# Kernel tuning notes

Hardware: AMD Instinct MI355X
Metric: run time of the kernel (lower is better)

## Reference

```python
import jax, jax.numpy as jnp
import numpy as np

B, TOK, NT = 64, 64, 456          # batch, token_encoder_dim, num gene tokens
T = NT * TOK                      # flat gene_exp dim = 29184
D, H, NL = 256, 8, 4              # d_model, nhead, num_layers
HD = D // H                       # head_dim = 32
FF = 4 * D                        # ffn hidden
PH = 32                           # attention-pooling hidden
L = NT + 1                        # seq len incl. CLS token
LN_EPS = 1e-5
BN_EPS = 1e-5


def build_alibi_slopes(n_heads):
    # faithful to FlashAttentionBlock.build_alibi_slopes (base=2.0)
    return jnp.array([1.0 / 2.0 ** (i // (n_heads / 2.0)) for i in range(n_heads)],
                     dtype=jnp.float32)


def _ln(x, g, b):
    m = jnp.mean(x, axis=-1, keepdims=True)
    v = jnp.mean(jnp.square(x - m), axis=-1, keepdims=True)
    return (x - m) * jax.lax.rsqrt(v + LN_EPS) * g + b


def setup_inputs() -> dict:
    key = jax.random.key(0)
    ks = jax.random.split(key, 24)
    s = 0.02
    return {
        "gene_exp": jax.random.normal(ks[0], (B, T), dtype=jnp.float32),
        "coords": jax.random.normal(ks[1], (B, 3), dtype=jnp.float32),
        "w_in": jax.random.normal(ks[2], (TOK, D)) * s,
        "b_in": jnp.zeros((D,), jnp.float32),
        "w_cls": jax.random.normal(ks[3], (3, D)) * s,
        "b_cls": jnp.zeros((D,), jnp.float32),
        "qkv_w": jax.random.normal(ks[4], (NL, D, 3 * D)) * s,
        "qkv_b": jnp.zeros((NL, 3 * D), jnp.float32),
        "ln1_g": jnp.ones((NL, D), jnp.float32),
        "ln1_b": jnp.zeros((NL, D), jnp.float32),
        "ffn_w1": jax.random.normal(ks[5], (NL, D, FF)) * s,
        "ffn_b1": jnp.zeros((NL, FF), jnp.float32),
        "ffn_w2": jax.random.normal(ks[6], (NL, FF, D)) * s,
        "ffn_b2": jnp.zeros((NL, D), jnp.float32),
        "ln2_g": jnp.ones((NL, D), jnp.float32),
        "ln2_b": jnp.zeros((NL, D), jnp.float32),
        "th1_w": jax.random.normal(ks[7], (D, PH)) * s,
        "th1_b": jnp.zeros((PH,), jnp.float32),
        "bn_g": jnp.ones((PH,), jnp.float32),
        "bn_b": jnp.zeros((PH,), jnp.float32),
        "th2_w": jax.random.normal(ks[8], (PH, 1)) * s,
        "th2_b": jnp.zeros((1,), jnp.float32),
    }


def reference(gene_exp, coords, w_in, b_in, w_cls, b_cls, qkv_w, qkv_b,
              ln1_g, ln1_b, ffn_w1, ffn_b1, ffn_w2, ffn_b2, ln2_g, ln2_b,
              th1_w, th1_b, bn_g, bn_b, th2_w, th2_b):
    # tokenize gene expression + project
    x = gene_exp.reshape(B, NT, TOK) @ w_in + b_in            # [B, NT, D]
    cls = (coords @ w_cls + b_cls)[:, None, :]                # [B, 1, D]
    x = jnp.concatenate([cls, x], axis=1)                     # [B, L, D]

    # ALiBi bias: -slope_h * |i - j| (non-causal flash-attn convention)
    slopes = build_alibi_slopes(H)                            # [H]
    pos = jnp.arange(L, dtype=jnp.float32)
    bias = -slopes[:, None, None] * jnp.abs(pos[:, None] - pos[None, :])  # [H,L,L]

    scale = 1.0 / np.sqrt(HD)
    for l in range(NL):
        residual = x
        qkv = (x @ qkv_w[l] + qkv_b[l]).reshape(B, L, 3, H, HD)
        q, k, v = qkv[:, :, 0], qkv[:, :, 1], qkv[:, :, 2]    # [B, L, H, HD]
        scores = jnp.einsum('bihd,bjhd->bhij', q, k) * scale + bias
        attn = jax.nn.softmax(scores, axis=-1)                # [B, H, L, L]
        out = jnp.einsum('bhij,bjhd->bihd', attn, v).reshape(B, L, D)
        x = _ln(residual + out, ln1_g[l], ln1_b[l])
        residual = x
        h = jax.nn.relu(x @ ffn_w1[l] + ffn_b1[l]) @ ffn_w2[l] + ffn_b2[l]
        x = _ln(residual + h, ln2_g[l], ln2_b[l])

    # AttentionPooling (BatchNorm1d in eval mode: running mean 0, var 1)
    h = x @ th1_w + th1_b                                     # [B, L, PH]
    h = h * (bn_g / np.sqrt(1.0 + BN_EPS)) + bn_b
    scores = jax.nn.gelu(h) @ th2_w + th2_b                   # [B, L, 1]
    attn_w = jax.nn.softmax(scores, axis=1)[..., 0]           # [B, L]
    pooled = jnp.einsum('bl,bld->bd', attn_w, x)              # [B, D]
    return pooled
```

## Files before the change

kernel.cpp:

```cpp
#include <hip/hip_runtime.h>
#include <math.h>

#define B_   64
#define TOK_ 64
#define NT_  456
#define L_   457
#define D_   256
#define H_   8
#define HD_  32
#define FF_  1024
#define NL_  4
#define PH_  32
#define MPAD 29312

typedef unsigned int uint;
typedef unsigned short ushort;
typedef __bf16 v8bf __attribute__((ext_vector_type(8)));
typedef __bf16 v4bf __attribute__((ext_vector_type(4)));
typedef short v4s __attribute__((ext_vector_type(4)));
typedef float v4f __attribute__((ext_vector_type(4)));

__device__ __forceinline__ float bu2f(ushort x) {
    return __uint_as_float(((uint)x) << 16);
}
__device__ __forceinline__ ushort f2bu(float f) {
    union { float f; uint u; } x; x.f = f;
    uint r = (x.u + 0x7fffu + ((x.u >> 16) & 1u)) >> 16;
    return (ushort)r;
}
__device__ __forceinline__ uint pack_bf2(float a, float b) {
#if defined(__HIP_DEVICE_COMPILE__) && __has_builtin(__builtin_amdgcn_cvt_pk_bf16_f32)
    typedef __bf16 bf2v __attribute__((ext_vector_type(2)));
    bf2v v = __builtin_amdgcn_cvt_pk_bf16_f32(a, b);
    return *(uint*)&v;
#else
    return (uint)f2bu(a) | ((uint)f2bu(b) << 16);
#endif
}

__device__ __forceinline__ v4f mfma16(uint2 a, uint2 b, v4f c) {
#if defined(__HIP_DEVICE_COMPILE__)
#if __has_builtin(__builtin_amdgcn_mfma_f32_16x16x16_bf16)
    return __builtin_amdgcn_mfma_f32_16x16x16_bf16(*(v4bf*)&a, *(v4bf*)&b, c, 0, 0, 0);
#else
    return __builtin_amdgcn_mfma_f32_16x16x16bf16_1k(*(v4s*)&a, *(v4s*)&b, c, 0, 0, 0);
#endif
#else
    (void)a; (void)b;
    return c;
#endif
}

__device__ __forceinline__ void gload16(const void* g, void* l) {
    __builtin_amdgcn_global_load_lds(
        (const __attribute__((address_space(1))) void*)(unsigned long long)(uintptr_t)g,
        (__attribute__((address_space(3))) void*)(uint)(uintptr_t)l,
        16, 0, 0);
}

__global__ __launch_bounds__(256) void mfma_gemm(
    const ushort* __restrict__ A, const ushort* __restrict__ WT,
    const float* __restrict__ bias, ushort* __restrict__ Cout,
    int N, int K, int relu, int T)
{
    __shared__ ushort lds_all[128 * 132];
    ushort* As = lds_all;
    ushort* Bs = lds_all + 128 * 64;

    int nCB = N >> 7;
    int per = gridDim.x >> 3;
    int lid = blockIdx.x;
    int nlid = (lid & 7) * per + (lid >> 3);
    if (nlid >= T) return;
    int colblk = (nlid % nCB) * 128;
    int rowblk = (nlid / nCB) * 128;

    int tid = threadIdx.x;
    int wave = tid >> 6, lane = tid & 63;
    int wm = wave >> 1, wn = wave & 1;
    int fr = lane & 15, fq = lane >> 4;

    v4f acc[4][4];
#pragma unroll
    for (int i = 0; i < 4; ++i)
#pragma unroll
        for (int j = 0; j < 4; ++j) acc[i][j] = (v4f)0.0f;

    const ushort* Ag[4];
    const ushort* Bg[4];
    ushort* lA[4];
    ushort* lB[4];
#pragma unroll
    for (int p = 0; p < 4; ++p) {
        int c = p * 256 + wave * 64 + lane;
        int r = c >> 3, gs = (c & 7) ^ (r & 7);
        Ag[p] = A + (size_t)(rowblk + r) * K + gs * 8;
        Bg[p] = WT + (size_t)(colblk + r) * K + gs * 8;
        lA[p] = As + (size_t)(p * 256 + wave * 64) * 8;
        lB[p] = Bs + (size_t)(p * 256 + wave * 64) * 8;
    }

    for (int kt = 0; kt < K; kt += 64) {
#pragma unroll
        for (int p = 0; p < 4; ++p) gload16(Ag[p] + kt, lA[p]);
#pragma unroll
        for (int p = 0; p < 4; ++p) gload16(Bg[p] + kt, lB[p]);
        __syncthreads();

#pragma unroll
        for (int ks = 0; ks < 2; ++ks) {
            int pa = (ks * 4 + fq) ^ (fr & 7);
            v8bf a[4], b[4];
#pragma unroll
            for (int mi = 0; mi < 4; ++mi) {
                int rl = wm * 64 + mi * 16 + fr;
                a[mi] = *(const v8bf*)(As + (size_t)(rl * 8 + pa) * 8);
            }
#pragma unroll
            for (int ni = 0; ni < 4; ++ni) {
                int rl = wn * 64 + ni * 16 + fr;
                b[ni] = *(const v8bf*)(Bs + (size_t)(rl * 8 + pa) * 8);
            }
#pragma unroll
            for (int mi = 0; mi < 4; ++mi)
#pragma unroll
                for (int ni = 0; ni < 4; ++ni)
                    acc[mi][ni] = __builtin_amdgcn_mfma_f32_16x16x32_bf16(
                        a[mi], b[ni], acc[mi][ni], 0, 0, 0);
        }
        __syncthreads();
    }

#pragma unroll
    for (int ni = 0; ni < 4; ++ni) {
        int col = wn * 64 + ni * 16 + fr;
        float bv = bias[colblk + col];
#pragma unroll
        for (int mi = 0; mi < 4; ++mi) {
            int row0 = wm * 64 + mi * 16 + fq * 4;
#pragma unroll
            for (int r = 0; r < 4; ++r) {
                float v = acc[mi][ni][r] + bv;
                if (relu) v = fmaxf(v, 0.f);
                lds_all[(size_t)(row0 + r) * 132 + col] = f2bu(v);
            }
        }
    }
    __syncthreads();
#pragma unroll
    for (int i = 0; i < 8; ++i) {
        int u = tid + 256 * i;
        int row = u >> 4, c8 = (u & 15) * 8;
        uint4 val = *(const uint4*)&lds_all[(size_t)row * 132 + c8];
        *(uint4*)(Cout + (size_t)(rowblk + row) * N + colblk + c8) = val;
    }
}

__global__ __launch_bounds__(256) void wcast_kernel(
    const float* __restrict__ W, ushort* __restrict__ WT, int K, int N)
{
    __shared__ float t[32][33];
    const float* Wl = W + (size_t)blockIdx.z * K * N;
    ushort* WTl = WT + (size_t)blockIdx.z * K * N;
    int n0 = blockIdx.x * 32, k0 = blockIdx.y * 32;
    int tx = threadIdx.x, ty = threadIdx.y;
#pragma unroll
    for (int r = 0; r < 32; r += 8)
        t[ty + r][tx] = Wl[(size_t)(k0 + ty + r) * N + n0 + tx];
    __syncthreads();
#pragma unroll
    for (int r = 0; r < 32; r += 8)
        WTl[(size_t)(n0 + ty + r) * K + k0 + tx] = f2bu(t[tx][ty + r]);
}

__global__ __launch_bounds__(256) void sgemm_kernel(
    const float* __restrict__ A, const float* __restrict__ W,
    const float* __restrict__ bias, ushort* __restrict__ Cb,
    int M, int N, int K)
{
    __shared__ float As_[16][64];
    __shared__ float Bs_[16][64];
    int tid = threadIdx.x;
    int rowblk = blockIdx.y * 64;
    int colblk = blockIdx.x * 64;
    int a_row = tid & 63, a_q = tid >> 6;
    int b_kr = tid >> 4, b_cg = tid & 15;
    int rm = tid >> 4, cn = tid & 15;
    float acc[4][4] = {};
    const float* Aptr = A + (size_t)(rowblk + a_row) * K;
    for (int kt = 0; kt < K; kt += 16) {
        float4 av = *(const float4*)(Aptr + kt + a_q * 4);
        float4 bv = *(const float4*)(W + (size_t)(kt + b_kr) * N + colblk + b_cg * 4);
        As_[a_q * 4 + 0][a_row] = av.x;
        As_[a_q * 4 + 1][a_row] = av.y;
        As_[a_q * 4 + 2][a_row] = av.z;
        As_[a_q * 4 + 3][a_row] = av.w;
        *(float4*)&Bs_[b_kr][b_cg * 4] = bv;
        __syncthreads();
#pragma unroll
        for (int kk = 0; kk < 16; ++kk) {
            float4 a4 = *(const float4*)&As_[kk][rm * 4];
            float4 b4 = *(const float4*)&Bs_[kk][cn * 4];
            float ar[4] = {a4.x, a4.y, a4.z, a4.w};
            float br[4] = {b4.x, b4.y, b4.z, b4.w};
#pragma unroll
            for (int i = 0; i < 4; ++i)
#pragma unroll
                for (int j = 0; j < 4; ++j) acc[i][j] += ar[i] * br[j];
        }
        __syncthreads();
    }
    float4 bv = *(const float4*)(bias + colblk + cn * 4);
    float bb[4] = {bv.x, bv.y, bv.z, bv.w};
#pragma unroll
    for (int i = 0; i < 4; ++i) {
        int grow = rowblk + rm * 4 + i;
        size_t orow = (size_t)(grow + grow / NT_ + 1);
        ushort4 h;
        h.x = f2bu(acc[i][0] + bb[0]);
        h.y = f2bu(acc[i][1] + bb[1]);
        h.z = f2bu(acc[i][2] + bb[2]);
        h.w = f2bu(acc[i][3] + bb[3]);
        *(ushort4*)(Cb + orow * N + colblk + cn * 4) = h;
    }
}

__global__ __launch_bounds__(256) void cls_kernel(
    const float* __restrict__ coords, const float* __restrict__ w_cls,
    const float* __restrict__ b_cls, ushort* __restrict__ Xb)
{
    int b = blockIdx.x;
    int t = threadIdx.x;
    float c0 = coords[b * 3 + 0], c1 = coords[b * 3 + 1], c2 = coords[b * 3 + 2];
    float v = c0 * w_cls[t] + c1 * w_cls[D_ + t] + c2 * w_cls[2 * D_ + t] + b_cls[t];
    Xb[(size_t)b * L_ * D_ + t] = f2bu(v);
}

__global__ __launch_bounds__(512) void attn_kernel(
    const ushort* __restrict__ qkv, ushort* __restrict__ out)
{
    __shared__ __align__(16) ushort Ks[464][40];
    __shared__ __align__(16) ushort Vt[32][488];

    int h = blockIdx.x, b = blockIdx.y;
    int tid = threadIdx.x;
    int wave = tid >> 6, lane = tid & 63;
    int fr = lane & 15, fq = lane >> 4;
    const float scale2 = 0.17677669529663687f * 1.4426950408889634f;
    float slope2 = ((h < 4) ? 1.0f : 0.5f) * 1.4426950408889634f;
    int W = (h < 4) ? 32 : 64;
    const ushort* base = qkv + (size_t)b * L_ * 768;

    for (int j = tid >> 2; j < 464; j += 128) {
        int c8 = (tid & 3) * 8;
        uint4 u = make_uint4(0u, 0u, 0u, 0u);
        if (j < L_) u = *(const uint4*)(base + (size_t)j * 768 + 256 + h * 32 + c8);
        *(uint4*)&Ks[j][c8] = u;
    }
    for (int m = wave; m < 32; m += 8) {
        int dg = (m >> 3) * 8, jb = m & 7;
        int j = jb * 64 + lane;
        uint4 u = make_uint4(0u, 0u, 0u, 0u);
        if (j < L_) u = *(const uint4*)(base + (size_t)j * 768 + 512 + h * 32 + dg);
        if (j < 488) {
            const ushort* pu = (const ushort*)&u;
#pragma unroll
            for (int e = 0; e < 8; ++e) Vt[dg + e][j] = pu[e];
        }
    }
    __syncthreads();

    for (int pr = wave; pr < 15; pr += 8) {
        int q0 = pr * 32;
        int twoB = (pr < 14);
        int kclo = max(0, (q0 - W) >> 5);
        int kchi = min(13, (q0 + 31 + W) >> 5);
        int doTail = (q0 + 31 + W >= 448);
        uint4 quA = *(const uint4*)(base + (size_t)(q0 + fr) * 768 + h * 32 + fq * 8);
        v8bf qfA = *(v8bf*)&quA;
        uint4 quB = *(const uint4*)(base + (size_t)(q0 + 16 + fr) * 768 + h * 32 + fq * 8);
        v8bf qfB = *(v8bf*)&quB;
        float fqAq = (float)(q0 + fr);
        float fqBq = fqAq + 16.0f;
        float psA = 0.f, psB = 0.f;
        v4f oA0 = (v4f)0.0f, oA1 = (v4f)0.0f, oB0 = (v4f)0.0f, oB1 = (v4f)0.0f;

        for (int kc = kclo; kc <= kchi; ++kc) {
            int kb = kc * 32;
            v8bf kf0 = *(const v8bf*)&Ks[kb + fr][fq * 8];
            v8bf kf1 = *(const v8bf*)&Ks[kb + 16 + fr][fq * 8];
            uint2 va0 = *(const uint2*)&Vt[fr][kb + fq * 4];
            uint2 va1 = *(const uint2*)&Vt[16 + fr][kb + fq * 4];
            uint2 vb0 = *(const uint2*)&Vt[fr][kb + 16 + fq * 4];
            uint2 vb1 = *(const uint2*)&Vt[16 + fr][kb + 16 + fq * 4];
            float ke = (float)(kb + 4 * fq);

            v4f dA0 = (v4f)0.0f, dA1 = (v4f)0.0f;
            dA0 = __builtin_amdgcn_mfma_f32_16x16x32_bf16(kf0, qfA, dA0, 0, 0, 0);
            dA1 = __builtin_amdgcn_mfma_f32_16x16x32_bf16(kf1, qfA, dA1, 0, 0, 0);
            {
                float dl0 = fqAq - ke, dl1 = dl0 - 16.0f;
                float pe[4], po[4];
#pragma unroll
                for (int r = 0; r < 4; ++r) {
                    pe[r] = exp2f(fmaf(dA0[r], scale2, -slope2 * fabsf(dl0 - (float)r)));
                    po[r] = exp2f(fmaf(dA1[r], scale2, -slope2 * fabsf(dl1 - (float)r)));
                    psA += pe[r] + po[r];
                }
                uint2 ue, uo;
                ue.x = pack_bf2(pe[0], pe[1]); ue.y = pack_bf2(pe[2], pe[3]);
                uo.x = pack_bf2(po[0], po[1]); uo.y = pack_bf2(po[2], po[3]);
                oA0 = mfma16(va0, ue, oA0);
                oA1 = mfma16(va1, ue, oA1);
                oA0 = mfma16(vb0, uo, oA0);
                oA1 = mfma16(vb1, uo, oA1);
            }
            if (twoB) {
                v4f dB0 = (v4f)0.0f, dB1 = (v4f)0.0f;
                dB0 = __builtin_amdgcn_mfma_f32_16x16x32_bf16(kf0, qfB, dB0, 0, 0, 0);
                dB1 = __builtin_amdgcn_mfma_f32_16x16x32_bf16(kf1, qfB, dB1, 0, 0, 0);
                float dl0 = fqBq - ke, dl1 = dl0 - 16.0f;
                float pe[4], po[4];
#pragma unroll
                for (int r = 0; r < 4; ++r) {
                    pe[r] = exp2f(fmaf(dB0[r], scale2, -slope2 * fabsf(dl0 - (float)r)));
                    po[r] = exp2f(fmaf(dB1[r], scale2, -slope2 * fabsf(dl1 - (float)r)));
                    psB += pe[r] + po[r];
                }
                uint2 ue, uo;
                ue.x = pack_bf2(pe[0], pe[1]); ue.y = pack_bf2(pe[2], pe[3]);
                uo.x = pack_bf2(po[0], po[1]); uo.y = pack_bf2(po[2], po[3]);
                oB0 = mfma16(va0, ue, oB0);
                oB1 = mfma16(va1, ue, oB1);
                oB0 = mfma16(vb0, uo, oB0);
                oB1 = mfma16(vb1, uo, oB1);
            }
        }
        if (doTail) {
            v8bf kf0 = *(const v8bf*)&Ks[448 + fr][fq * 8];
            uint2 va0 = *(const uint2*)&Vt[fr][448 + fq * 4];
            uint2 va1 = *(const uint2*)&Vt[16 + fr][448 + fq * 4];
            v4f dA0 = (v4f)0.0f;
            dA0 = __builtin_amdgcn_mfma_f32_16x16x32_bf16(kf0, qfA, dA0, 0, 0, 0);
            float pe[4];
#pragma unroll
            for (int r = 0; r < 4; ++r) {
                int k = 448 + 4 * fq + r;
                pe[r] = (k < L_)
                    ? exp2f(fmaf(dA0[r], scale2, -slope2 * fabsf(fqAq - (float)k))) : 0.f;
                psA += pe[r];
            }
            uint2 ue;
            ue.x = pack_bf2(pe[0], pe[1]); ue.y = pack_bf2(pe[2], pe[3]);
            oA0 = mfma16(va0, ue, oA0);
            oA1 = mfma16(va1, ue, oA1);
            if (twoB) {
                v4f dB0 = (v4f)0.0f;
                dB0 = __builtin_amdgcn_mfma_f32_16x16x32_bf16(kf0, qfB, dB0, 0, 0, 0);
                float pf[4];
#pragma unroll
                for (int r = 0; r < 4; ++r) {
                    int k = 448 + 4 * fq + r;
                    pf[r] = (k < L_)
                        ? exp2f(fmaf(dB0[r], scale2, -slope2 * fabsf(fqBq - (float)k))) : 0.f;
                    psB += pf[r];
                }
                uint2 ub;
                ub.x = pack_bf2(pf[0], pf[1]); ub.y = pack_bf2(pf[2], pf[3]);
                oB0 = mfma16(va0, ub, oB0);
                oB1 = mfma16(va1, ub, oB1);
            }
        }

        psA += __shfl_xor(psA, 16);
        psA += __shfl_xor(psA, 32);
        psB += __shfl_xor(psB, 16);
        psB += __shfl_xor(psB, 32);
        {
            int q = q0 + fr;
            if (q < L_) {
                float inv = 1.0f / psA;
                uint2 w0, w1;
                w0.x = pack_bf2(oA0[0] * inv, oA0[1] * inv);
                w0.y = pack_bf2(oA0[2] * inv, oA0[3] * inv);
                w1.x = pack_bf2(oA1[0] * inv, oA1[1] * inv);
                w1.y = pack_bf2(oA1[2] * inv, oA1[3] * inv);
                ushort* op = out + (size_t)(b * L_ + q) * D_ + h * 32;
                *(uint2*)(op + fq * 4) = w0;
                *(uint2*)(op + 16 + fq * 4) = w1;
            }
        }
        if (twoB) {
            int q = q0 + 16 + fr;
            if (q < L_) {
                float inv = 1.0f / psB;
                uint2 w0, w1;
                w0.x = pack_bf2(oB0[0] * inv, oB0[1] * inv);
                w0.y = pack_bf2(oB0[2] * inv, oB0[3] * inv);
                w1.x = pack_bf2(oB1[0] * inv, oB1[1] * inv);
                w1.y = pack_bf2(oB1[2] * inv, oB1[3] * inv);
                ushort* op = out + (size_t)(b * L_ + q) * D_ + h * 32;
                *(uint2*)(op + fq * 4) = w0;
                *(uint2*)(op + 16 + fq * 4) = w1;
            }
        }
    }
}

__global__ __launch_bounds__(256) void ln_kernel(
    const ushort* __restrict__ res, const ushort* __restrict__ y,
    const float* __restrict__ g, const float* __restrict__ bb,
    ushort* __restrict__ xbout)
{
    int row = blockIdx.x * 4 + (threadIdx.x >> 6);
    int lane = threadIdx.x & 63;
    size_t off = (size_t)row * D_ + lane * 4;
    ushort4 rv4 = *(const ushort4*)(res + off);
    ushort4 yv4 = *(const ushort4*)(y + off);
    float4 v;
    v.x = bu2f(rv4.x) + bu2f(yv4.x);
    v.y = bu2f(rv4.y) + bu2f(yv4.y);
    v.z = bu2f(rv4.z) + bu2f(yv4.z);
    v.w = bu2f(rv4.w) + bu2f(yv4.w);

    float s = v.x + v.y + v.z + v.w;
#pragma unroll
    for (int o = 1; o < 64; o <<= 1) s += __shfl_xor(s, o);
    float mean = s * (1.0f / 256.0f);

    float4 d;
    d.x = v.x - mean; d.y = v.y - mean; d.z = v.z - mean; d.w = v.w - mean;
    float sq = d.x * d.x + d.y * d.y + d.z * d.z + d.w * d.w;
#pragma unroll
    for (int o = 1; o < 64; o <<= 1) sq += __shfl_xor(sq, o);
    float rstd = rsqrtf(sq * (1.0f / 256.0f) + 1e-5f);

    float4 gv = *(const float4*)(g + lane * 4);
    float4 bv = *(const float4*)(bb + lane * 4);
    ushort4 hb;
    hb.x = f2bu(d.x * rstd * gv.x + bv.x);
    hb.y = f2bu(d.y * rstd * gv.y + bv.y);
    hb.z = f2bu(d.z * rstd * gv.z + bv.z);
    hb.w = f2bu(d.w * rstd * gv.w + bv.w);
    *(ushort4*)(xbout + off) = hb;
}

__global__ __launch_bounds__(256) void head1_kernel(
    const ushort* __restrict__ Xb, const ushort* __restrict__ th1T,
    const float* __restrict__ b1, const float* __restrict__ bng,
    const float* __restrict__ bnb, const float* __restrict__ w2,
    const float* __restrict__ b2, float* __restrict__ SCp)
{
    __shared__ ushort As[128 * 32];
    __shared__ ushort Bs[32 * 264];
    int tid = threadIdx.x;
    int wave = tid >> 6, lane = tid & 63;
    int fr = lane & 15, fq = lane >> 4;
    int rowblk = blockIdx.x * 128;
    int scol = fq ^ (lane & 3) ^ ((lane >> 2) & 1);

    for (int i = tid; i < 1024; i += 256) {
        int r = i >> 5, c8 = (i & 31) * 8;
        *(uint4*)&Bs[r * 264 + c8] = *(const uint4*)(th1T + r * 256 + c8);
    }

    int c0 = wave * 64 + lane;
    int r0 = c0 >> 2, k0g = (c0 & 3) ^ (r0 & 3) ^ ((r0 >> 2) & 1);
    int c1 = 256 + c0;
    int r1 = c1 >> 2, k1g = (c1 & 3) ^ (r1 & 3) ^ ((r1 >> 2) & 1);
    const ushort* Ag0 = Xb + (size_t)(rowblk + r0) * 256 + k0g * 8;
    const ushort* Ag1 = Xb + (size_t)(rowblk + r1) * 256 + k1g * 8;
    ushort* lA0 = As + (size_t)(wave * 64) * 8;
    ushort* lA1 = As + (size_t)(256 + wave * 64) * 8;

    v4f acc[2][2];
#pragma unroll
    for (int i = 0; i < 2; ++i)
#pragma unroll
        for (int j = 0; j < 2; ++j) acc[i][j] = (v4f)0.0f;

    for (int kt = 0; kt < 256; kt += 32) {
        gload16(Ag0 + kt, lA0);
        gload16(Ag1 + kt, lA1);
        __syncthreads();
        v8bf a[2], bfr[2];
#pragma unroll
        for (int mi = 0; mi < 2; ++mi)
            a[mi] = *(const v8bf*)(As + (size_t)((wave * 2 + mi) * 16 + fr) * 32 + scol * 8);
#pragma unroll
        for (int ni = 0; ni < 2; ++ni)
            bfr[ni] = *(const v8bf*)(Bs + (size_t)(ni * 16 + fr) * 264 + kt + fq * 8);
#pragma unroll
        for (int mi = 0; mi < 2; ++mi)
#pragma unroll
            for (int ni = 0; ni < 2; ++ni)
                acc[mi][ni] = __builtin_amdgcn_mfma_f32_16x16x32_bf16(
                    a[mi], bfr[ni], acc[mi][ni], 0, 0, 0);
        __syncthreads();
    }

    const float bnr = 0.9999950000374997f;
    float b1v[2], bsv[2], bbv[2], w2v[2];
#pragma unroll
    for (int ni = 0; ni < 2; ++ni) {
        int j = ni * 16 + fr;
        b1v[ni] = b1[j];
        bsv[ni] = bng[j] * bnr;
        bbv[ni] = bnb[j];
        w2v[ni] = w2[j];
    }
    const float gc = 0.7978845608028654f;
    float b2v = b2[0];
#pragma unroll
    for (int mi = 0; mi < 2; ++mi) {
#pragma unroll
        for (int r = 0; r < 4; ++r) {
            float s = 0.f;
#pragma unroll
            for (int ni = 0; ni < 2; ++ni) {
                float hb = (acc[mi][ni][r] + b1v[ni]) * bsv[ni] + bbv[ni];
                float t = tanhf(gc * (hb + 0.044715f * hb * hb * hb));
                s += 0.5f * hb * (1.0f + t) * w2v[ni];
            }
#pragma unroll
            for (int o = 1; o < 16; o <<= 1) s += __shfl_xor(s, o);
            int row = rowblk + (wave * 2 + mi) * 16 + fq * 4 + r;
            if (fr == 0 && row < B_ * L_) SCp[row] = s + b2v;
        }
    }
}

__global__ __launch_bounds__(256) void head2_kernel(
    const float* __restrict__ SCp, const ushort* __restrict__ Xb,
    float* __restrict__ outp)
{
    int cg = blockIdx.x, b = blockIdx.y;
    int tid = threadIdx.x;
    __shared__ float wbuf[L_];
    __shared__ float r1[4], r2[4];
    __shared__ float part[4][64];
    const float* s = SCp + (size_t)b * L_;

    float m = -1e30f;
    for (int j = tid; j < L_; j += 256) m = fmaxf(m, s[j]);
#pragma unroll
    for (int o = 1; o < 64; o <<= 1) m = fmaxf(m, __shfl_xor(m, o));
    if ((tid & 63) == 0) r1[tid >> 6] = m;
    __syncthreads();
    m = fmaxf(fmaxf(r1[0], r1[1]), fmaxf(r1[2], r1[3]));

    float sum = 0.f;
    for (int j = tid; j < L_; j += 256) {
        float e = __expf(s[j] - m);
        wbuf[j] = e;
        sum += e;
    }
#pragma unroll
    for (int o = 1; o < 64; o <<= 1) sum += __shfl_xor(sum, o);
    if ((tid & 63) == 0) r2[tid >> 6] = sum;
    __syncthreads();
    float inv = 1.0f / (r2[0] + r2[1] + r2[2] + r2[3]);

    int c = tid & 63, pt = tid >> 6;
    int col = cg * 64 + c;
    float acc = 0.f;
    const ushort* xb = Xb + (size_t)b * L_ * D_ + col;
    for (int l = pt; l < L_; l += 4) acc += wbuf[l] * bu2f(xb[(size_t)l * D_]);
    part[pt][c] = acc;
    __syncthreads();
    if (pt == 0)
        outp[b * D_ + col] = (part[0][c] + part[1][c] + part[2][c] + part[3][c]) * inv;
}

extern "C" void kernel_launch(void* const* d_in, const int* in_sizes, int n_in,
                              void* d_out, int out_size, void* d_ws, size_t ws_size,
                              hipStream_t stream)
{
    const float* gene   = (const float*)d_in[0];
    const float* coords = (const float*)d_in[1];
    const float* w_in   = (const float*)d_in[2];
    const float* b_in   = (const float*)d_in[3];
    const float* w_cls  = (const float*)d_in[4];
    const float* b_cls  = (const float*)d_in[5];
    const float* qkv_w  = (const float*)d_in[6];
    const float* qkv_b  = (const float*)d_in[7];
    const float* ln1_g  = (const float*)d_in[8];
    const float* ln1_b  = (const float*)d_in[9];
    const float* ffn_w1 = (const float*)d_in[10];
    const float* ffn_b1 = (const float*)d_in[11];
    const float* ffn_w2 = (const float*)d_in[12];
    const float* ffn_b2 = (const float*)d_in[13];
    const float* ln2_g  = (const float*)d_in[14];
    const float* ln2_b  = (const float*)d_in[15];
    const float* th1_w  = (const float*)d_in[16];
    const float* th1_b  = (const float*)d_in[17];
    const float* bn_g   = (const float*)d_in[18];
    const float* bn_b   = (const float*)d_in[19];
    const float* th2_w  = (const float*)d_in[20];
    const float* th2_b  = (const float*)d_in[21];
    float* out = (float*)d_out;

    const int ROWS = B_ * L_;
    char* p = (char*)d_ws;
    ushort* AOb  = (ushort*)p; p += (size_t)MPAD * 256 * 2;
    ushort* Xb   = (ushort*)p; p += (size_t)MPAD * 256 * 2;
    ushort* SH   = (ushort*)p; p += (size_t)MPAD * 1024 * 2;
    ushort* qkvT = (ushort*)p; p += (size_t)NL_ * 768 * 256 * 2;
    ushort* w1T  = (ushort*)p; p += (size_t)NL_ * 1024 * 256 * 2;
    ushort* w2T  = (ushort*)p; p += (size_t)NL_ * 256 * 1024 * 2;
    ushort* th1T = (ushort*)p; p += (size_t)32 * 256 * 2;
    float*  SCp  = (float*)p;  p += (size_t)ROWS * 4;

    const int RB = MPAD / 128;
    const int Tqkv = (768 / 128) * RB;
    const int Tff1 = (1024 / 128) * RB;
    const int Tff2 = (256 / 128) * RB;
    const int Pqkv = (Tqkv + 7) & ~7;
    const int Pff1 = (Tff1 + 7) & ~7;
    const int Pff2 = (Tff2 + 7) & ~7;

    wcast_kernel<<<dim3(768 / 32, 256 / 32, NL_), dim3(32, 8), 0, stream>>>(qkv_w, qkvT, 256, 768);
    wcast_kernel<<<dim3(1024 / 32, 256 / 32, NL_), dim3(32, 8), 0, stream>>>(ffn_w1, w1T, 256, 1024);
    wcast_kernel<<<dim3(256 / 32, 1024 / 32, NL_), dim3(32, 8), 0, stream>>>(ffn_w2, w2T, 1024, 256);
    wcast_kernel<<<dim3(1, 8, 1), dim3(32, 8), 0, stream>>>(th1_w, th1T, 256, 32);

    sgemm_kernel<<<dim3(D_ / 64, (B_ * NT_) / 64), 256, 0, stream>>>(
        gene, w_in, b_in, Xb, B_ * NT_, D_, TOK_);
    cls_kernel<<<B_, 256, 0, stream>>>(coords, w_cls, b_cls, Xb);

    for (int l = 0; l < NL_; ++l) {
        mfma_gemm<<<Pqkv, 256, 0, stream>>>(
            Xb, qkvT + (size_t)l * 768 * 256, qkv_b + l * 768, SH, 768, 256, 0, Tqkv);
        attn_kernel<<<dim3(H_, B_), 512, 0, stream>>>(SH, AOb);
        ln_kernel<<<ROWS / 4, 256, 0, stream>>>(Xb, AOb, ln1_g + l * D_, ln1_b + l * D_, Xb);
        mfma_gemm<<<Pff1, 256, 0, stream>>>(
            Xb, w1T + (size_t)l * 1024 * 256, ffn_b1 + l * 1024, SH, 1024, 256, 1, Tff1);
        mfma_gemm<<<Pff2, 256, 0, stream>>>(
            SH, w2T + (size_t)l * 256 * 1024, ffn_b2 + l * D_, AOb, 256, 1024, 0, Tff2);
        ln_kernel<<<ROWS / 4, 256, 0, stream>>>(Xb, AOb, ln2_g + l * D_, ln2_b + l * D_, Xb);
    }

    head1_kernel<<<MPAD / 128, 256, 0, stream>>>(
        Xb, th1T, th1_b, bn_g, bn_b, th2_w, th2_b, SCp);
    head2_kernel<<<dim3(4, B_), 256, 0, stream>>>(SCp, Xb, out);
}
```

Measured before the change: 704.6 us.

## Rewrite MFMA GEMM as 256x128 tile with triple-buffered async LDS pipeline

Replaces the 128x128, 256-thread GEMM with a 512-thread kernel that computes 256x128 tiles. It streams K in 32-wide chunks through a three-slot LDS ring, using global_load_lds prefetch two steps ahead. Each step uses a single barrier with manual vmcnt waits and raises wave priority around the MFMA block. It also changes the XCD-aware block remapping and pads MPAD to a multiple of 256. The aim is to hide global-load latency and halve the barrier count per K step. In exchange it uses more LDS and registers per block, which can lower occupancy.

```diff
diff --git a/kernel.cpp b/kernel.cpp
--- a/kernel.cpp
+++ b/kernel.cpp
@@ -11,7 +11,7 @@
 #define FF_  1024
 #define NL_  4
 #define PH_  32
-#define MPAD 29312
+#define MPAD 29440
 
 typedef unsigned int uint;
 typedef unsigned short ushort;
@@ -58,101 +58,130 @@
         16, 0, 0);
 }
 
-__global__ __launch_bounds__(256) void mfma_gemm(
+__global__ __launch_bounds__(512, 2) void mfma_gemm8(
     const ushort* __restrict__ A, const ushort* __restrict__ WT,
     const float* __restrict__ bias, ushort* __restrict__ Cout,
-    int N, int K, int relu, int T)
-{
-    __shared__ ushort lds_all[128 * 132];
-    ushort* As = lds_all;
-    ushort* Bs = lds_all + 128 * 64;
-
+    int N, int K, int relu)
+{
+    __shared__ ushort lds[36864];
+
+    const int NK = K >> 5;
+
+    int nwg = gridDim.x, orig = blockIdx.x;
+    int qd = nwg >> 3, rd = nwg & 7;
+    int xcd = orig & 7, wi = orig >> 3;
+    int wgid = (xcd < rd ? xcd * (qd + 1) : rd * (qd + 1) + (xcd - rd) * qd) + wi;
     int nCB = N >> 7;
-    int per = gridDim.x >> 3;
-    int lid = blockIdx.x;
-    int nlid = (lid & 7) * per + (lid >> 3);
-    if (nlid >= T) return;
-    int colblk = (nlid % nCB) * 128;
-    int rowblk = (nlid / nCB) * 128;
+    int colblk = (wgid % nCB) << 7;
+    int rowblk = (wgid / nCB) << 8;
 
     int tid = threadIdx.x;
     int wave = tid >> 6, lane = tid & 63;
     int wm = wave >> 1, wn = wave & 1;
     int fr = lane & 15, fq = lane >> 4;
 
+    const ushort* srcA0; const ushort* srcA1; const ushort* srcB0;
+    {
+        int idx = tid;
+        int c = idx >> 3, G = (idx & 7) ^ (c & 7);
+        srcA0 = A + (size_t)(rowblk + c * 2 + (G >> 2)) * K + (G & 3) * 8;
+        idx = 512 + tid;
+        c = idx >> 3; G = (idx & 7) ^ (c & 7);
+        srcA1 = A + (size_t)(rowblk + c * 2 + (G >> 2)) * K + (G & 3) * 8;
+        idx = tid;
+        c = idx >> 3; G = (idx & 7) ^ (c & 7);
+        srcB0 = WT + (size_t)(colblk + c * 2 + (G >> 2)) * K + (G & 3) * 8;
+    }
+    int duA0 = (wave * 64) * 8;
+    int duA1 = (512 + wave * 64) * 8;
+    int duB  = (wave * 64) * 8;
+
+    int aoff[4], boff[4];
+#pragma unroll
+    for (int i = 0; i < 4; ++i) {
+        int rl = wm * 64 + i * 16 + fr;
+        int c = rl >> 1;
+        aoff[i] = c * 64 + ((((rl & 1) * 4 + fq) ^ (c & 7)) * 8);
+        rl = wn * 64 + i * 16 + fr;
+        c = rl >> 1;
+        boff[i] = c * 64 + ((((rl & 1) * 4 + fq) ^ (c & 7)) * 8);
+    }
+
     v4f acc[4][4];
 #pragma unroll
     for (int i = 0; i < 4; ++i)
 #pragma unroll
         for (int j = 0; j < 4; ++j) acc[i][j] = (v4f)0.0f;
 
-    const ushort* Ag[4];
-    const ushort* Bg[4];
-    ushort* lA[4];
-    ushort* lB[4];
-#pragma unroll
-    for (int p = 0; p < 4; ++p) {
-        int c = p * 256 + wave * 64 + lane;
-        int r = c >> 3, gs = (c & 7) ^ (r & 7);
-        Ag[p] = A + (size_t)(rowblk + r) * K + gs * 8;
-        Bg[p] = WT + (size_t)(colblk + r) * K + gs * 8;
-        lA[p] = As + (size_t)(p * 256 + wave * 64) * 8;
-        lB[p] = Bs + (size_t)(p * 256 + wave * 64) * 8;
-    }
-
-    for (int kt = 0; kt < K; kt += 64) {
-#pragma unroll
-        for (int p = 0; p < 4; ++p) gload16(Ag[p] + kt, lA[p]);
-#pragma unroll
-        for (int p = 0; p < 4; ++p) gload16(Bg[p] + kt, lB[p]);
+#pragma unroll
+    for (int t = 0; t < 2; ++t) {
+        ushort* pa = lds + t * 8192;
+        ushort* pb = lds + 24576 + t * 4096;
+        gload16(srcA0 + t * 32, pa + duA0);
+        gload16(srcA1 + t * 32, pa + duA1);
+        gload16(srcB0 + t * 32, pb + duB);
+    }
+
+    for (int t = 0; t < NK; ++t) {
+        int slot = t % 3, pslot = (t + 2) % 3;
+        const ushort* As = lds + slot * 8192;
+        const ushort* Bs = lds + 24576 + slot * 4096;
+
+        if (t < NK - 1) asm volatile("s_waitcnt vmcnt(3)" ::: "memory");
+        else            asm volatile("s_waitcnt vmcnt(0)" ::: "memory");
+        __builtin_amdgcn_s_barrier();
+        asm volatile("" ::: "memory");
+
+        if (t + 2 < NK) {
+            ushort* pa = lds + pslot * 8192;
+            ushort* pb = lds + 24576 + pslot * 4096;
+            gload16(srcA0 + (t + 2) * 32, pa + duA0);
+            gload16(srcA1 + (t + 2) * 32, pa + duA1);
+            gload16(srcB0 + (t + 2) * 32, pb + duB);
+        }
+
+        v8bf av[4], bw[4];
+#pragma unroll
+        for (int i = 0; i < 4; ++i) av[i] = *(const v8bf*)(As + aoff[i]);
+#pragma unroll
+        for (int i = 0; i < 4; ++i) bw[i] = *(const v8bf*)(Bs + boff[i]);
+
+        __builtin_amdgcn_s_setprio(1);
+#pragma unroll
+        for (int mi = 0; mi < 4; ++mi)
+#pragma unroll
+            for (int ni = 0; ni < 4; ++ni)
+                acc[mi][ni] = __builtin_amdgcn_mfma_f32_16x16x32_bf16(
+                    av[mi], bw[ni], acc[mi][ni], 0, 0, 0);
+        __builtin_amdgcn_s_setprio(0);
+    }
+
+    __syncthreads();
+    {
+        const int PIT = 136;
+#pragma unroll
+        for (int ni = 0; ni < 4; ++ni) {
+            int col = wn * 64 + ni * 16 + fr;
+            float bv = bias[colblk + col];
+#pragma unroll
+            for (int mi = 0; mi < 4; ++mi) {
+                int row0 = wm * 64 + mi * 16 + fq * 4;
+#pragma unroll
+                for (int r2 = 0; r2 < 4; ++r2) {
+                    float v = acc[mi][ni][r2] + bv;
+                    if (relu) v = fmaxf(v, 0.f);
+                    lds[(row0 + r2) * PIT + col] = f2bu(v);
+                }
+            }
+        }
         __syncthreads();
-
-#pragma unroll
-        for (int ks = 0; ks < 2; ++ks) {
-            int pa = (ks * 4 + fq) ^ (fr & 7);
-            v8bf a[4], b[4];
-#pragma unroll
-            for (int mi = 0; mi < 4; ++mi) {
-                int rl = wm * 64 + mi * 16 + fr;
-                a[mi] = *(const v8bf*)(As + (size_t)(rl * 8 + pa) * 8);
-            }
-#pragma unroll
-            for (int ni = 0; ni < 4; ++ni) {
-                int rl = wn * 64 + ni * 16 + fr;
-                b[ni] = *(const v8bf*)(Bs + (size_t)(rl * 8 + pa) * 8);
-            }
-#pragma unroll
-            for (int mi = 0; mi < 4; ++mi)
-#pragma unroll
-                for (int ni = 0; ni < 4; ++ni)
-                    acc[mi][ni] = __builtin_amdgcn_mfma_f32_16x16x32_bf16(
-                        a[mi], b[ni], acc[mi][ni], 0, 0, 0);
-        }
-        __syncthreads();
-    }
-
-#pragma unroll
-    for (int ni = 0; ni < 4; ++ni) {
-        int col = wn * 64 + ni * 16 + fr;
-        float bv = bias[colblk + col];
-#pragma unroll
-        for (int mi = 0; mi < 4; ++mi) {
-            int row0 = wm * 64 + mi * 16 + fq * 4;
-#pragma unroll
-            for (int r = 0; r < 4; ++r) {
-                float v = acc[mi][ni][r] + bv;
-                if (relu) v = fmaxf(v, 0.f);
-                lds_all[(size_t)(row0 + r) * 132 + col] = f2bu(v);
-            }
-        }
-    }
-    __syncthreads();
-#pragma unroll
-    for (int i = 0; i < 8; ++i) {
-        int u = tid + 256 * i;
-        int row = u >> 4, c8 = (u & 15) * 8;
-        uint4 val = *(const uint4*)&lds_all[(size_t)row * 132 + c8];
-        *(uint4*)(Cout + (size_t)(rowblk + row) * N + colblk + c8) = val;
+#pragma unroll
+        for (int i = 0; i < 8; ++i) {
+            int u = tid + 512 * i;
+            int row = u >> 4, c8 = (u & 15) * 8;
+            uint4 val = *(const uint4*)&lds[row * PIT + c8];
+            *(uint4*)(Cout + (size_t)(rowblk + row) * N + colblk + c8) = val;
+        }
     }
 }
 
@@ -611,13 +640,7 @@
     ushort* th1T = (ushort*)p; p += (size_t)32 * 256 * 2;
     float*  SCp  = (float*)p;  p += (size_t)ROWS * 4;
 
-    const int RB = MPAD / 128;
-    const int Tqkv = (768 / 128) * RB;
-    const int Tff1 = (1024 / 128) * RB;
-    const int Tff2 = (256 / 128) * RB;
-    const int Pqkv = (Tqkv + 7) & ~7;
-    const int Pff1 = (Tff1 + 7) & ~7;
-    const int Pff2 = (Tff2 + 7) & ~7;
+    const int RB2 = MPAD / 256;
 
     wcast_kernel<<<dim3(768 / 32, 256 / 32, NL_), dim3(32, 8), 0, stream>>>(qkv_w, qkvT, 256, 768);
     wcast_kernel<<<dim3(1024 / 32, 256 / 32, NL_), dim3(32, 8), 0, stream>>>(ffn_w1, w1T, 256, 1024);
@@ -629,14 +652,14 @@
     cls_kernel<<<B_, 256, 0, stream>>>(coords, w_cls, b_cls, Xb);
 
     for (int l = 0; l < NL_; ++l) {
-        mfma_gemm<<<Pqkv, 256, 0, stream>>>(
-            Xb, qkvT + (size_t)l * 768 * 256, qkv_b + l * 768, SH, 768, 256, 0, Tqkv);
+        mfma_gemm8<<<RB2 * (768 / 128), 512, 0, stream>>>(
+            Xb, qkvT + (size_t)l * 768 * 256, qkv_b + l * 768, SH, 768, 256, 0);
         attn_kernel<<<dim3(H_, B_), 512, 0, stream>>>(SH, AOb);
         ln_kernel<<<ROWS / 4, 256, 0, stream>>>(Xb, AOb, ln1_g + l * D_, ln1_b + l * D_, Xb);
-        mfma_gemm<<<Pff1, 256, 0, stream>>>(
-            Xb, w1T + (size_t)l * 1024 * 256, ffn_b1 + l * 1024, SH, 1024, 256, 1, Tff1);
-        mfma_gemm<<<Pff2, 256, 0, stream>>>(
-            SH, w2T + (size_t)l * 256 * 1024, ffn_b2 + l * D_, AOb, 256, 1024, 0, Tff2);
+        mfma_gemm8<<<RB2 * (1024 / 128), 512, 0, stream>>>(
+            Xb, w1T + (size_t)l * 1024 * 256, ffn_b1 + l * 1024, SH, 1024, 256, 1);
+        mfma_gemm8<<<RB2 * (256 / 128), 512, 0, stream>>>(
+            SH, w2T + (size_t)l * 256 * 1024, ffn_b2 + l * D_, AOb, 256, 1024, 0);
         ln_kernel<<<ROWS / 4, 256, 0, stream>>>(Xb, AOb, ln2_g + l * D_, ln2_b + l * D_, Xb);
     }
 
```

Measured after the change: 662.5 us. -6.0%, faster.
